# Performance work log

Measured on AMD Instinct MI355X. Metric: run time of the kernel, lower is better.

The kernel has to match this reference:

```python
import jax, jax.numpy as jnp
import numpy as np

NEG_SLOPE = 0.2
N_NODES = 50000
N_EDGES = 800000
IN_DIM = 256
HID_DIM = 256
HEADS = 8
HEAD_DIM = HID_DIM // HEADS


def setup_inputs() -> dict:
    key = jax.random.key(0)
    ks = jax.random.split(key, 12)
    def glorot(k, shape):
        fan = sum(shape[-2:]) if len(shape) > 1 else shape[-1] + 1
        return jax.random.normal(k, shape, jnp.float32) * jnp.sqrt(2.0 / fan)
    return {
        "data": jax.random.normal(ks[0], (N_NODES, IN_DIM), jnp.float32),
        "src": jax.random.randint(ks[1], (N_EDGES,), 0, N_NODES),
        "dst": jax.random.randint(ks[2], (N_EDGES,), 0, N_NODES),
        "W1": glorot(ks[3], (IN_DIM, HID_DIM)),
        "al1": glorot(ks[4], (HEADS, HEAD_DIM)),
        "ar1": glorot(ks[5], (HEADS, HEAD_DIM)),
        "b1": jnp.zeros((HID_DIM,), jnp.float32),
        "W2": glorot(ks[6], (HID_DIM, HID_DIM)),
        "al2": glorot(ks[7], (HEADS, HEAD_DIM)),
        "ar2": glorot(ks[8], (HEADS, HEAD_DIM)),
        "b2": jnp.zeros((HID_DIM,), jnp.float32),
    }


def gat_layer(x, src, dst, W, al, ar, b):
    """One DGL-style GATConv layer with ReLU activation."""
    N = x.shape[0]
    feat = (x @ W).reshape(N, HEADS, HEAD_DIM)            # [N,H,D]
    el = jnp.sum(feat * al[None], axis=-1)                # [N,H]
    er = jnp.sum(feat * ar[None], axis=-1)                # [N,H]
    e = el[src] + er[dst]                                  # [E,H]
    e = jnp.where(e > 0, e, NEG_SLOPE * e)                 # LeakyReLU(0.2)
    # segment softmax over incoming edges of each dst node
    m = jax.ops.segment_max(e, dst, num_segments=N)        # [N,H] (-inf for empty)
    a = jnp.exp(e - m[dst])                                # [E,H]
    denom = jax.ops.segment_sum(a, dst, num_segments=N)    # [N,H]
    alpha = a / denom[dst]                                 # [E,H]
    msg = feat[src] * alpha[:, :, None]                    # [E,H,D]
    out = jax.ops.segment_sum(msg, dst, num_segments=N)    # [N,H,D]
    out = out + b.reshape(1, HEADS, HEAD_DIM)
    out = jax.nn.relu(out)
    return out.reshape(N, HID_DIM)


def reference(data, src, dst, W1, al1, ar1, b1, W2, al2, ar2, b2):
    h = gat_layer(data, src, dst, W1, al1, ar1, b1)
    h = gat_layer(h, src, dst, W2, al2, ar2, b2)
    return h
```

## Files before the change

### kernel.cpp

```cpp
#include <hip/hip_runtime.h>

#define N_NODES 50000
#define N_EDGES 800000
#define DIM 256
#define HEADS 8
#define NEG_SLOPE 0.2f
#define MAXDEG 64
#define OVFCAP 65536

typedef unsigned short u16;
typedef float floatx4 __attribute__((ext_vector_type(4)));
typedef __bf16 bf16x8 __attribute__((ext_vector_type(8)));

__device__ __forceinline__ float b2f(u16 u) {
    union { unsigned int i; float f; } v; v.i = ((unsigned int)u) << 16; return v.f;
}
__device__ __forceinline__ u16 f2b(float f) {
    union { float f; unsigned int i; } v; v.f = f;
    unsigned int x = v.i;
    if ((x & 0x7f800000u) == 0x7f800000u && (x & 0x007fffffu)) {
        return (u16)((x >> 16) | 0x0040u);
    }
    unsigned int r = (x + 0x7fffu + ((x >> 16) & 1u)) >> 16;
    return (u16)r;
}

__global__ __launch_bounds__(256) void fill_u32(unsigned int* __restrict__ p,
                                                unsigned int v, int n) {
    int i = blockIdx.x * 256 + threadIdx.x;
    if (i < n) p[i] = v;
}

__global__ __launch_bounds__(256) void init_kernel(const unsigned int* __restrict__ d,
                                                   int* __restrict__ counts,
                                                   int* __restrict__ flag,
                                                   int* __restrict__ novf) {
    int i = blockIdx.x * 256 + threadIdx.x;
    if (i < N_NODES) counts[i] = 0;
    if (blockIdx.x == 0) {
        __shared__ int cnt;
        if (threadIdx.x == 0) { cnt = 0; *novf = 0; }
        __syncthreads();
        unsigned int w = d[threadIdx.x];
        int bad = 0;
        #pragma unroll
        for (int half = 0; half < 2; ++half) {
            u16 u = (u16)(w >> (16 * half));
            unsigned int e = (u >> 7) & 0xFFu;
            if (u != 0 && (e >= 141u || e <= 27u)) bad = 1;
        }
        atomicAdd(&cnt, bad);
        __syncthreads();
        if (threadIdx.x == 0) *flag = (cnt > 64) ? 1 : 0;
    }
}

__global__ __launch_bounds__(256) void prep_kernel(const void* __restrict__ W1,
                                                   const void* __restrict__ W2,
                                                   u16* __restrict__ Wt1,
                                                   u16* __restrict__ Wt2,
                                                   const int* __restrict__ flagp) {
    const int isf = *flagp;
    int b = blockIdx.x;
    const void* W = (b < 16) ? W1 : W2;
    u16* Wt = (b < 16) ? Wt1 : Wt2;
    int t = b & 15;
    int k0 = (t >> 2) * 64, n0 = (t & 3) * 64;
    __shared__ float lt[64][65];
    int c = threadIdx.x & 63, r0 = threadIdx.x >> 6;
    #pragma unroll
    for (int j = 0; j < 16; ++j) {
        int r = j * 4 + r0;
        lt[r][c] = isf ? ((const float*)W)[(k0 + r) * 256 + n0 + c]
                       : b2f(((const u16*)W)[(k0 + r) * 256 + n0 + c]);
    }
    __syncthreads();
    #pragma unroll
    for (int j = 0; j < 16; ++j) {
        int rn = j * 4 + r0;
        Wt[(n0 + rn) * 256 + k0 + c] = f2b(lt[c][rn]);
    }
}

__global__ __launch_bounds__(256) void build_kernel(const int* __restrict__ src,
                                                    const int* __restrict__ dst,
                                                    int* __restrict__ counts,
                                                    int* __restrict__ padded,
                                                    int* __restrict__ novf,
                                                    int2* __restrict__ ovf, int E) {
    int i = blockIdx.x * 256 + threadIdx.x;
    if (i < E) {
        int d = dst[i];
        int s = src[i];
        int pos = atomicAdd(&counts[d], 1);
        if (pos < MAXDEG) {
            padded[d * MAXDEG + pos] = s;
        } else {
            int oi = atomicAdd(novf, 1);
            if (oi < OVFCAP) { int2 pr; pr.x = d; pr.y = s; ovf[oi] = pr; }
        }
    }
}

__global__ __launch_bounds__(256) void hist_kernel(const int* __restrict__ dst,
                                                   int* __restrict__ counts, int E) {
    int i = blockIdx.x * 256 + threadIdx.x;
    if (i < E) atomicAdd(&counts[dst[i]], 1);
}

__global__ __launch_bounds__(256) void scan_partial(const int* __restrict__ counts,
                                                    int* __restrict__ partial, int n) {
    int b = blockIdx.x, tid = threadIdx.x;
    int base = b * 1024 + tid * 4;
    int s = 0;
    #pragma unroll
    for (int k = 0; k < 4; ++k) if (base + k < n) s += counts[base + k];
    int lane = tid & 63;
    #pragma unroll
    for (int off = 32; off; off >>= 1) s += __shfl_xor(s, off);
    __shared__ int wsum[4];
    if (lane == 0) wsum[tid >> 6] = s;
    __syncthreads();
    if (tid == 0) partial[b] = wsum[0] + wsum[1] + wsum[2] + wsum[3];
}

__global__ __launch_bounds__(64) void scan_offsets(const int* __restrict__ partial,
                                                   int* __restrict__ offsets,
                                                   int* __restrict__ row_ptr,
                                                   int nb, int n) {
    int t = threadIdx.x;
    int v0 = (t < nb) ? partial[t] : 0;
    int v = v0;
    #pragma unroll
    for (int d = 1; d < 64; d <<= 1) {
        int u = __shfl_up(v, d);
        if (t >= d) v += u;
    }
    if (t < nb) offsets[t] = v - v0;
    if (t == 63) row_ptr[n] = v;
}

__global__ __launch_bounds__(256) void scan_write(const int* __restrict__ counts,
                                                  const int* __restrict__ offsets,
                                                  int* __restrict__ row_ptr,
                                                  int* __restrict__ wptr, int n) {
    int b = blockIdx.x, tid = threadIdx.x;
    int base = b * 1024 + tid * 4;
    int v[4]; int s = 0;
    #pragma unroll
    for (int k = 0; k < 4; ++k) { v[k] = (base + k < n) ? counts[base + k] : 0; s += v[k]; }
    int lane = tid & 63, w = tid >> 6;
    int incl = s;
    #pragma unroll
    for (int d = 1; d < 64; d <<= 1) {
        int u = __shfl_up(incl, d);
        if (lane >= d) incl += u;
    }
    __shared__ int wsum[4];
    if (lane == 63) wsum[w] = incl;
    __syncthreads();
    int woff = 0;
    for (int i = 0; i < w; ++i) woff += wsum[i];
    int run = offsets[b] + woff + incl - s;
    #pragma unroll
    for (int k = 0; k < 4; ++k) {
        if (base + k < n) { row_ptr[base + k] = run; wptr[base + k] = run; run += v[k]; }
    }
}

__global__ __launch_bounds__(256) void scatter_kernel(const int* __restrict__ src,
                                                      const int* __restrict__ dst,
                                                      int* __restrict__ wptr,
                                                      int* __restrict__ src_sorted, int E) {
    int i = blockIdx.x * 256 + threadIdx.x;
    if (i < E) {
        int pos = atomicAdd(&wptr[dst[i]], 1);
        src_sorted[pos] = src[i];
    }
}

#define LDA 264

__global__ __launch_bounds__(256, 3) void gemm_fused(const void* __restrict__ Araw,
                                                     int maybe_f32,
                                                     const u16* __restrict__ Wt,
                                                     u16* __restrict__ outF,
                                                     float* __restrict__ el,
                                                     float* __restrict__ er,
                                                     const void* __restrict__ al,
                                                     const void* __restrict__ ar,
                                                     int M, const int* __restrict__ flagp) {
    const int isf = *flagp;
    const bool af32 = (maybe_f32 != 0) && (isf != 0);
    __shared__ u16 As[64][LDA];
    const int tid  = threadIdx.x;
    const int w    = tid >> 6;
    const int lane = tid & 63;
    const int quad = lane >> 4;
    const int l16  = lane & 15;
    const int m0   = blockIdx.x * 64;

    const u16* wbase = Wt + (size_t)(64 * w + l16) * 256 + quad * 8;

    bf16x8 bCur[4], bNxt[4], aCur[4], aNxt[4];
    #pragma unroll
    for (int t = 0; t < 4; ++t)
        bCur[t] = *(const bf16x8*)(wbase + (size_t)t * 16 * 256);

    if (af32) {
        const float* Af = (const float*)Araw;
        #pragma unroll
        for (int it = 0; it < 8; ++it) {
            int idx = it * 256 + tid;
            int r = idx >> 5;
            int c = (idx & 31) << 3;
            int gr = m0 + r;
            u16 tb[8];
            if (gr < M) {
                float4 f0 = *(const float4*)(Af + (size_t)gr * 256 + c);
                float4 f1 = *(const float4*)(Af + (size_t)gr * 256 + c + 4);
                tb[0] = f2b(f0.x); tb[1] = f2b(f0.y); tb[2] = f2b(f0.z); tb[3] = f2b(f0.w);
                tb[4] = f2b(f1.x); tb[5] = f2b(f1.y); tb[6] = f2b(f1.z); tb[7] = f2b(f1.w);
            } else {
                #pragma unroll
                for (int k = 0; k < 8; ++k) tb[k] = 0;
            }
            *(uint4*)&As[r][c] = *(uint4*)tb;
        }
    } else {
        const u16* Ab = (const u16*)Araw;
        #pragma unroll
        for (int it = 0; it < 8; ++it) {
            int idx = it * 256 + tid;
            int r = idx >> 5;
            int c = (idx & 31) << 3;
            int gr = m0 + r;
            if (gr < M) {
                *(uint4*)&As[r][c] = *(const uint4*)(Ab + (size_t)gr * 256 + c);
            } else {
                uint4 z = {0u, 0u, 0u, 0u};
                *(uint4*)&As[r][c] = z;
            }
        }
    }
    __syncthreads();

    #pragma unroll
    for (int i = 0; i < 4; ++i)
        aCur[i] = *(const bf16x8*)&As[16 * i + l16][quad * 8];

    floatx4 acc[4][4] = {};

    #pragma unroll
    for (int s = 0; s < 8; ++s) {
        if (s < 7) {
            #pragma unroll
            for (int t = 0; t < 4; ++t)
                bNxt[t] = *(const bf16x8*)(wbase + (size_t)t * 16 * 256 + (s + 1) * 32);
            #pragma unroll
            for (int i = 0; i < 4; ++i)
                aNxt[i] = *(const bf16x8*)&As[16 * i + l16][(s + 1) * 32 + quad * 8];
        }
        #pragma unroll
        for (int i = 0; i < 4; ++i)
            #pragma unroll
            for (int t = 0; t < 4; ++t)
                acc[i][t] = __builtin_amdgcn_mfma_f32_16x16x32_bf16(aCur[i], bCur[t], acc[i][t], 0, 0, 0);
        if (s < 7) {
            #pragma unroll
            for (int t = 0; t < 4; ++t) bCur[t] = bNxt[t];
            #pragma unroll
            for (int i = 0; i < 4; ++i) aCur[i] = aNxt[i];
        }
    }

    __syncthreads();
    u16* Ct = (u16*)As;
    #pragma unroll
    for (int i = 0; i < 4; ++i)
        #pragma unroll
        for (int t = 0; t < 4; ++t) {
            int col = 64 * w + 16 * t + l16;
            #pragma unroll
            for (int r = 0; r < 4; ++r)
                Ct[(16 * i + quad * 4 + r) * LDA + col] = f2b(acc[i][t][r]);
        }
    __syncthreads();
    #pragma unroll
    for (int it = 0; it < 4; ++it) {
        int idx = it * 256 + tid;
        int row = idx >> 4;
        int c16 = (idx & 15) * 16;
        int gr = m0 + row;
        if (gr < M) {
            uint4 v0 = *(const uint4*)&Ct[row * LDA + c16];
            uint4 v1 = *(const uint4*)&Ct[row * LDA + c16 + 8];
            *(uint4*)(outF + (size_t)gr * 256 + c16) = v0;
            *(uint4*)(outF + (size_t)gr * 256 + c16 + 8) = v1;
        }
    }

    float alv[4], arv[4];
    #pragma unroll
    for (int t = 0; t < 4; ++t) {
        int c = 64 * w + 16 * t + l16;
        alv[t] = isf ? ((const float*)al)[c] : b2f(((const u16*)al)[c]);
        arv[t] = isf ? ((const float*)ar)[c] : b2f(((const u16*)ar)[c]);
    }
    #pragma unroll
    for (int i = 0; i < 4; ++i)
        #pragma unroll
        for (int r = 0; r < 4; ++r) {
            int row = m0 + 16 * i + quad * 4 + r;
            #pragma unroll
            for (int tt = 0; tt < 2; ++tt) {
                float pl = acc[i][2 * tt][r] * alv[2 * tt] + acc[i][2 * tt + 1][r] * alv[2 * tt + 1];
                float pr = acc[i][2 * tt][r] * arv[2 * tt] + acc[i][2 * tt + 1][r] * arv[2 * tt + 1];
                #pragma unroll
                for (int mask = 1; mask <= 8; mask <<= 1) {
                    pl += __shfl_xor(pl, mask);
                    pr += __shfl_xor(pr, mask);
                }
                if (l16 == 0 && row < M) {
                    el[row * 8 + 2 * w + tt] = pl;
                    er[row * 8 + 2 * w + tt] = pr;
                }
            }
        }
}

__global__ __launch_bounds__(256) void aggregate_kernel(const u16* __restrict__ feat,
                                                        const float* __restrict__ el,
                                                        const float* __restrict__ er,
                                                        const void* __restrict__ bias,
                                                        const int* __restrict__ idxinfo,
                                                        const int* __restrict__ srcbuf,
                                                        void* __restrict__ out,
                                                        int out_mode,
                                                        int node0,
                                                        const int* __restrict__ flagp,
                                                        int pmode,
                                                        const int* __restrict__ novfp,
                                                        const int2* __restrict__ ovf) {
    const int isf = *flagp;
    const int lane = threadIdx.x & 63;
    const int node = node0 + blockIdx.x * 4 + (threadIdx.x >> 6);
    if (node >= N_NODES) return;
    const int h = lane >> 3;
    const int j = lane & 7;
    int beg, deg;
    if (pmode) { beg = node * MAXDEG; deg = idxinfo[node]; }
    else       { beg = idxinfo[node]; deg = idxinfo[node + 1] - beg; }
    const int dcap = (pmode && deg > MAXDEG) ? MAXDEG : deg;
    int nov = 0;
    if (pmode && deg > MAXDEG) { nov = *novfp; if (nov > OVFCAP) nov = OVFCAP; }
    const float ern = er[node * HEADS + h];

    float m0v = -1e30f, ss0 = 0.f;
    float m1v = -1e30f, ss1 = 0.f;
    for (int i = j; i < dcap; i += 16) {
        int s0 = srcbuf[beg + i];
        int i2 = i + 8;
        int s1 = (i2 < dcap) ? srcbuf[beg + i2] : 0;
        float e0 = el[s0 * 8 + h] + ern;
        float e1 = el[s1 * 8 + h] + ern;
        e0 = e0 > 0.f ? e0 : NEG_SLOPE * e0;
        e1 = e1 > 0.f ? e1 : NEG_SLOPE * e1;
        if (i2 >= dcap) e1 = -3e30f;
        float mn0 = fmaxf(m0v, e0);
        ss0 = ss0 * __expf(m0v - mn0) + __expf(e0 - mn0);
        m0v = mn0;
        float mn1 = fmaxf(m1v, e1);
        ss1 = ss1 * __expf(m1v - mn1) + __expf(e1 - mn1);
        m1v = mn1;
    }
    for (int k = j; k < nov; k += 8) {
        int2 pr = ovf[k];
        if (pr.x != node) continue;
        float e = el[pr.y * 8 + h] + ern;
        e = e > 0.f ? e : NEG_SLOPE * e;
        float mn = fmaxf(m0v, e);
        ss0 = ss0 * __expf(m0v - mn) + __expf(e - mn);
        m0v = mn;
    }
    float m = fmaxf(m0v, m1v);
    float ssum = ss0 * __expf(m0v - m) + ss1 * __expf(m1v - m);
    #pragma unroll
    for (int mask = 1; mask <= 4; mask <<= 1) {
        float mo = __shfl_xor(m, mask);
        float so = __shfl_xor(ssum, mask);
        float mn = fmaxf(m, mo);
        ssum = ssum * __expf(m - mn) + so * __expf(mo - mn);
        m = mn;
    }
    const float mx = m;
    const float inv = ssum > 0.f ? 1.f / ssum : 0.f;

    const int q = lane & 31;
    const int half = lane >> 5;
    const int hq = q >> 2;
    float a[8] = {};

    int sC = 0; float avC = 0.f;
    if (j < dcap) {
        sC = srcbuf[beg + j];
        float e = el[sC * 8 + h] + ern;
        e = e > 0.f ? e : NEG_SLOPE * e;
        avC = __expf(e - mx) * inv;
    }
    uint4 f[4]; float ae[4];
    #pragma unroll
    for (int u = 0; u < 4; ++u) {
        int sel = hq * 8 + 2 * u + half;
        int se = __shfl(sC, sel);
        ae[u] = __shfl(avC, sel);
        f[u] = *(const uint4*)(feat + (size_t)se * DIM + 8 * q);
    }

    #pragma unroll 2
    for (int c0 = 0; c0 < dcap; c0 += 8) {
        uint4 f2[4]; float ae2[4];
        {
            int sN = 0; float avN = 0.f;
            int i = c0 + 8 + j;
            if (i < dcap) {
                sN = srcbuf[beg + i];
                float e = el[sN * 8 + h] + ern;
                e = e > 0.f ? e : NEG_SLOPE * e;
                avN = __expf(e - mx) * inv;
            }
            #pragma unroll
            for (int u = 0; u < 4; ++u) {
                int sel = hq * 8 + 2 * u + half;
                int se = __shfl(sN, sel);
                ae2[u] = __shfl(avN, sel);
                f2[u] = *(const uint4*)(feat + (size_t)se * DIM + 8 * q);
            }
        }
        #pragma unroll
        for (int u = 0; u < 4; ++u) {
            float wgt = ae[u];
            a[0] += wgt * b2f((u16)(f[u].x & 0xffffu)); a[1] += wgt * b2f((u16)(f[u].x >> 16));
            a[2] += wgt * b2f((u16)(f[u].y & 0xffffu)); a[3] += wgt * b2f((u16)(f[u].y >> 16));
            a[4] += wgt * b2f((u16)(f[u].z & 0xffffu)); a[5] += wgt * b2f((u16)(f[u].z >> 16));
            a[6] += wgt * b2f((u16)(f[u].w & 0xffffu)); a[7] += wgt * b2f((u16)(f[u].w >> 16));
        }
        #pragma unroll
        for (int u = 0; u < 4; ++u) { f[u] = f2[u]; ae[u] = ae2[u]; }
    }

    if (nov) {
        const float mxq  = __shfl(mx, hq * 8);
        const float invq = __shfl(inv, hq * 8);
        const float ernq = __shfl(ern, hq * 8);
        for (int k = 0; k < nov; ++k) {
            int2 pr = ovf[k];
            if (pr.x != node) continue;
            float av = 0.f;
            if (half == 0) {
                float e = el[pr.y * 8 + hq] + ernq;
                e = e > 0.f ? e : NEG_SLOPE * e;
                av = __expf(e - mxq) * invq;
            }
            uint4 fv = *(const uint4*)(feat + (size_t)pr.y * DIM + 8 * q);
            a[0] += av * b2f((u16)(fv.x & 0xffffu)); a[1] += av * b2f((u16)(fv.x >> 16));
            a[2] += av * b2f((u16)(fv.y & 0xffffu)); a[3] += av * b2f((u16)(fv.y >> 16));
            a[4] += av * b2f((u16)(fv.z & 0xffffu)); a[5] += av * b2f((u16)(fv.z >> 16));
            a[6] += av * b2f((u16)(fv.w & 0xffffu)); a[7] += av * b2f((u16)(fv.w >> 16));
        }
    }

    #pragma unroll
    for (int k = 0; k < 8; ++k) a[k] += __shfl_xor(a[k], 32);

    if (half == 0) {
        float o[8];
        if (isf) {
            float4 b0 = *(const float4*)((const float*)bias + 8 * q);
            float4 b1 = *(const float4*)((const float*)bias + 8 * q + 4);
            o[0] = a[0] + b0.x; o[1] = a[1] + b0.y; o[2] = a[2] + b0.z; o[3] = a[3] + b0.w;
            o[4] = a[4] + b1.x; o[5] = a[5] + b1.y; o[6] = a[6] + b1.z; o[7] = a[7] + b1.w;
        } else {
            uint4 bu = *(const uint4*)((const u16*)bias + 8 * q);
            o[0] = a[0] + b2f((u16)(bu.x & 0xffffu)); o[1] = a[1] + b2f((u16)(bu.x >> 16));
            o[2] = a[2] + b2f((u16)(bu.y & 0xffffu)); o[3] = a[3] + b2f((u16)(bu.y >> 16));
            o[4] = a[4] + b2f((u16)(bu.z & 0xffffu)); o[5] = a[5] + b2f((u16)(bu.z >> 16));
            o[6] = a[6] + b2f((u16)(bu.w & 0xffffu)); o[7] = a[7] + b2f((u16)(bu.w >> 16));
        }
        #pragma unroll
        for (int k = 0; k < 8; ++k) o[k] = fmaxf(o[k], 0.f);
        if (out_mode == 0 || !isf) {
            u16 pk[8] = {f2b(o[0]), f2b(o[1]), f2b(o[2]), f2b(o[3]),
                         f2b(o[4]), f2b(o[5]), f2b(o[6]), f2b(o[7])};
            *(uint4*)((u16*)out + (size_t)node * DIM + 8 * q) = *(uint4*)pk;
        } else {
            float4 v0 = {o[0], o[1], o[2], o[3]};
            float4 v1 = {o[4], o[5], o[6], o[7]};
            *(float4*)((float*)out + (size_t)node * DIM + 8 * q) = v0;
            *(float4*)((float*)out + (size_t)node * DIM + 8 * q + 4) = v1;
        }
    }
}

extern "C" void kernel_launch(void* const* d_in, const int* in_sizes, int n_in,
                              void* d_out, int out_size, void* d_ws, size_t ws_size,
                              hipStream_t stream) {
    const void* data = d_in[0];
    const int* src = (const int*)d_in[1];
    const int* dst = (const int*)d_in[2];
    const void* W1  = d_in[3];
    const void* al1 = d_in[4];
    const void* ar1 = d_in[5];
    const void* b1  = d_in[6];
    const void* W2  = d_in[7];
    const void* al2 = d_in[8];
    const void* ar2 = d_in[9];
    const void* b2  = d_in[10];

    const size_t BASE =
        (size_t)N_NODES * DIM * 2 +
        (size_t)N_NODES * HEADS * 4 * 2 +
        (size_t)N_NODES * 4 +
        2 * 256 * 256 * 2 +
        1024;
    const size_t NEEDED_PAD = BASE + (size_t)N_NODES * MAXDEG * 4 + (size_t)OVFCAP * 8;
    const size_t NEEDED_CSR = BASE + (size_t)N_NODES * 4 +
                              (size_t)(N_NODES + 4) * 4 +
                              (size_t)N_EDGES * 4;

    if (ws_size < NEEDED_CSR && ws_size < NEEDED_PAD) {
        int nwords = (out_size + 1) / 2;
        fill_u32<<<(nwords + 255) / 256, 256, 0, stream>>>(
            (unsigned int*)d_out, 0x42C842C8u, nwords);
        return;
    }

    char* ws = (char*)d_ws;
    u16* feat = (u16*)ws;        ws += (size_t)N_NODES * DIM * 2;
    float* el = (float*)ws;      ws += (size_t)N_NODES * HEADS * 4;
    float* er = (float*)ws;      ws += (size_t)N_NODES * HEADS * 4;
    int* counts = (int*)ws;      ws += (size_t)N_NODES * 4;
    u16* Wt1 = (u16*)ws;         ws += 256 * 256 * 2;
    u16* Wt2 = (u16*)ws;         ws += 256 * 256 * 2;
    int* flag = (int*)ws;        ws += 256;
    int* novf = (int*)ws;        ws += 256;
    int* partial = (int*)ws;     ws += 256;
    int* offsets = (int*)ws;     ws += 256;

    u16* h1 = (u16*)d_out;
    const int gemm_blocks = (N_NODES + 63) / 64;
    const int HALF = 25000;
    const int agg_half_blocks = HALF / 4;

    init_kernel<<<(N_NODES + 255) / 256, 256, 0, stream>>>(
        (const unsigned int*)data, counts, flag, novf);
    prep_kernel<<<32, 256, 0, stream>>>(W1, W2, Wt1, Wt2, flag);

    const int* idxinfo;
    const int* srcbuf;
    const int2* ovf = (const int2*)d_ws;
    int pmode;

    if (ws_size >= NEEDED_PAD) {
        int* padded = (int*)ws;  ws += (size_t)N_NODES * MAXDEG * 4;
        int2* ovfw = (int2*)ws;  ws += (size_t)OVFCAP * 8;
        build_kernel<<<(N_EDGES + 255) / 256, 256, 0, stream>>>(
            src, dst, counts, padded, novf, ovfw, N_EDGES);
        idxinfo = counts; srcbuf = padded; ovf = ovfw; pmode = 1;
    } else {
        int* wptr = (int*)ws;        ws += (size_t)N_NODES * 4;
        int* row_ptr = (int*)ws;     ws += (size_t)(N_NODES + 4) * 4;
        int* src_sorted = (int*)ws;  ws += (size_t)N_EDGES * 4;
        const int nb = (N_NODES + 1023) / 1024;
        hist_kernel<<<(N_EDGES + 255) / 256, 256, 0, stream>>>(dst, counts, N_EDGES);
        scan_partial<<<nb, 256, 0, stream>>>(counts, partial, N_NODES);
        scan_offsets<<<1, 64, 0, stream>>>(partial, offsets, row_ptr, nb, N_NODES);
        scan_write<<<nb, 256, 0, stream>>>(counts, offsets, row_ptr, wptr, N_NODES);
        scatter_kernel<<<(N_EDGES + 255) / 256, 256, 0, stream>>>(src, dst, wptr, src_sorted, N_EDGES);
        idxinfo = row_ptr; srcbuf = src_sorted; pmode = 0;
    }

    gemm_fused<<<gemm_blocks, 256, 0, stream>>>(data, 1, Wt1, feat,
                                                el, er, al1, ar1, N_NODES, flag);
    aggregate_kernel<<<agg_half_blocks, 256, 0, stream>>>(feat, el, er, b1, idxinfo, srcbuf,
                                                          (void*)h1, 0, 0, flag, pmode, novf, ovf);
    aggregate_kernel<<<agg_half_blocks, 256, 0, stream>>>(feat, el, er, b1, idxinfo, srcbuf,
                                                          (void*)h1, 0, HALF, flag, pmode, novf, ovf);
    gemm_fused<<<gemm_blocks, 256, 0, stream>>>(h1, 0, Wt2, feat,
                                                el, er, al2, ar2, N_NODES, flag);
    aggregate_kernel<<<agg_half_blocks, 256, 0, stream>>>(feat, el, er, b2, idxinfo, srcbuf,
                                                          d_out, 2, 0, flag, pmode, novf, ovf);
    aggregate_kernel<<<agg_half_blocks, 256, 0, stream>>>(feat, el, er, b2, idxinfo, srcbuf,
                                                          d_out, 2, HALF, flag, pmode, novf, ovf);
}
```

Measured before the change: 394.4 us.

## Vectorize edge build, drop LDS-staged GEMM store, merge split aggregate launches

```diff
diff --git a/kernel.cpp b/kernel.cpp
--- a/kernel.cpp
+++ b/kernel.cpp
@@ -88,16 +88,31 @@
                                                     int* __restrict__ padded,
                                                     int* __restrict__ novf,
                                                     int2* __restrict__ ovf, int E) {
-    int i = blockIdx.x * 256 + threadIdx.x;
-    if (i < E) {
-        int d = dst[i];
-        int s = src[i];
-        int pos = atomicAdd(&counts[d], 1);
-        if (pos < MAXDEG) {
-            padded[d * MAXDEG + pos] = s;
-        } else {
-            int oi = atomicAdd(novf, 1);
-            if (oi < OVFCAP) { int2 pr; pr.x = d; pr.y = s; ovf[oi] = pr; }
+    int base = blockIdx.x * 1024 + threadIdx.x * 4;
+    if (base + 3 < E) {
+        int4 d4 = *(const int4*)(dst + base);
+        int4 s4 = *(const int4*)(src + base);
+        int p0 = atomicAdd(&counts[d4.x], 1);
+        int p1 = atomicAdd(&counts[d4.y], 1);
+        int p2 = atomicAdd(&counts[d4.z], 1);
+        int p3 = atomicAdd(&counts[d4.w], 1);
+        if (p0 < MAXDEG) padded[d4.x * MAXDEG + p0] = s4.x;
+        else { int oi = atomicAdd(novf, 1); if (oi < OVFCAP) { int2 pr; pr.x = d4.x; pr.y = s4.x; ovf[oi] = pr; } }
+        if (p1 < MAXDEG) padded[d4.y * MAXDEG + p1] = s4.y;
+        else { int oi = atomicAdd(novf, 1); if (oi < OVFCAP) { int2 pr; pr.x = d4.y; pr.y = s4.y; ovf[oi] = pr; } }
+        if (p2 < MAXDEG) padded[d4.z * MAXDEG + p2] = s4.z;
+        else { int oi = atomicAdd(novf, 1); if (oi < OVFCAP) { int2 pr; pr.x = d4.z; pr.y = s4.z; ovf[oi] = pr; } }
+        if (p3 < MAXDEG) padded[d4.w * MAXDEG + p3] = s4.w;
+        else { int oi = atomicAdd(novf, 1); if (oi < OVFCAP) { int2 pr; pr.x = d4.w; pr.y = s4.w; ovf[oi] = pr; } }
+    } else {
+        for (int k = 0; k < 4; ++k) {
+            int i = base + k;
+            if (i < E) {
+                int d = dst[i], s = src[i];
+                int pos = atomicAdd(&counts[d], 1);
+                if (pos < MAXDEG) padded[d * MAXDEG + pos] = s;
+                else { int oi = atomicAdd(novf, 1); if (oi < OVFCAP) { int2 pr; pr.x = d; pr.y = s; ovf[oi] = pr; } }
+            }
         }
     }
 }
@@ -274,31 +289,15 @@
         }
     }
 
-    __syncthreads();
-    u16* Ct = (u16*)As;
     #pragma unroll
     for (int i = 0; i < 4; ++i)
         #pragma unroll
-        for (int t = 0; t < 4; ++t) {
-            int col = 64 * w + 16 * t + l16;
-            #pragma unroll
-            for (int r = 0; r < 4; ++r)
-                Ct[(16 * i + quad * 4 + r) * LDA + col] = f2b(acc[i][t][r]);
-        }
-    __syncthreads();
-    #pragma unroll
-    for (int it = 0; it < 4; ++it) {
-        int idx = it * 256 + tid;
-        int row = idx >> 4;
-        int c16 = (idx & 15) * 16;
-        int gr = m0 + row;
-        if (gr < M) {
-            uint4 v0 = *(const uint4*)&Ct[row * LDA + c16];
-            uint4 v1 = *(const uint4*)&Ct[row * LDA + c16 + 8];
-            *(uint4*)(outF + (size_t)gr * 256 + c16) = v0;
-            *(uint4*)(outF + (size_t)gr * 256 + c16 + 8) = v1;
-        }
-    }
+        for (int t = 0; t < 4; ++t)
+            #pragma unroll
+            for (int r = 0; r < 4; ++r) {
+                int row = m0 + 16 * i + quad * 4 + r;
+                if (row < M) outF[(size_t)row * 256 + 64 * w + 16 * t + l16] = f2b(acc[i][t][r]);
+            }
 
     float alv[4], arv[4];
     #pragma unroll
@@ -337,14 +336,13 @@
                                                         const int* __restrict__ srcbuf,
                                                         void* __restrict__ out,
                                                         int out_mode,
-                                                        int node0,
                                                         const int* __restrict__ flagp,
                                                         int pmode,
                                                         const int* __restrict__ novfp,
                                                         const int2* __restrict__ ovf) {
     const int isf = *flagp;
     const int lane = threadIdx.x & 63;
-    const int node = node0 + blockIdx.x * 4 + (threadIdx.x >> 6);
+    const int node = blockIdx.x * 4 + (threadIdx.x >> 6);
     if (node >= N_NODES) return;
     const int h = lane >> 3;
     const int j = lane & 7;
@@ -549,8 +547,7 @@
 
     u16* h1 = (u16*)d_out;
     const int gemm_blocks = (N_NODES + 63) / 64;
-    const int HALF = 25000;
-    const int agg_half_blocks = HALF / 4;
+    const int agg_blocks = (N_NODES + 3) / 4;
 
     init_kernel<<<(N_NODES + 255) / 256, 256, 0, stream>>>(
         (const unsigned int*)data, counts, flag, novf);
@@ -564,7 +561,7 @@
     if (ws_size >= NEEDED_PAD) {
         int* padded = (int*)ws;  ws += (size_t)N_NODES * MAXDEG * 4;
         int2* ovfw = (int2*)ws;  ws += (size_t)OVFCAP * 8;
-        build_kernel<<<(N_EDGES + 255) / 256, 256, 0, stream>>>(
+        build_kernel<<<(N_EDGES + 1023) / 1024, 256, 0, stream>>>(
             src, dst, counts, padded, novf, ovfw, N_EDGES);
         idxinfo = counts; srcbuf = padded; ovf = ovfw; pmode = 1;
     } else {
@@ -582,14 +579,10 @@
 
     gemm_fused<<<gemm_blocks, 256, 0, stream>>>(data, 1, Wt1, feat,
                                                 el, er, al1, ar1, N_NODES, flag);
-    aggregate_kernel<<<agg_half_blocks, 256, 0, stream>>>(feat, el, er, b1, idxinfo, srcbuf,
-                                                          (void*)h1, 0, 0, flag, pmode, novf, ovf);
-    aggregate_kernel<<<agg_half_blocks, 256, 0, stream>>>(feat, el, er, b1, idxinfo, srcbuf,
-                                                          (void*)h1, 0, HALF, flag, pmode, novf, ovf);
+    aggregate_kernel<<<agg_blocks, 256, 0, stream>>>(feat, el, er, b1, idxinfo, srcbuf,
+                                                     (void*)h1, 0, flag, pmode, novf, ovf);
     gemm_fused<<<gemm_blocks, 256, 0, stream>>>(h1, 0, Wt2, feat,
                                                 el, er, al2, ar2, N_NODES, flag);
-    aggregate_kernel<<<agg_half_blocks, 256, 0, stream>>>(feat, el, er, b2, idxinfo, srcbuf,
-                                                          d_out, 2, 0, flag, pmode, novf, ovf);
-    aggregate_kernel<<<agg_half_blocks, 256, 0, stream>>>(feat, el, er, b2, idxinfo, srcbuf,
-                                                          d_out, 2, HALF, flag, pmode, novf, ovf);
-}
+    aggregate_kernel<<<agg_blocks, 256, 0, stream>>>(feat, el, er, b2, idxinfo, srcbuf,
+                                                     d_out, 2, flag, pmode, novf, ovf);
+}
```

Result: faster. 375.4 us (-4.8%).
